# Kernel tuning notes

Measured on AMD Instinct MI355X. Metric: run time of the kernel, lower is better.

Reference implementation:

```python
import jax, jax.numpy as jnp
import numpy as np
import math

B, T, C, H = 4, 2048, 1024, 16
D = C // H  # head dim = 64


def setup_inputs() -> dict:
    key = jax.random.key(0)
    k1, k2, k3, k4, k5 = jax.random.split(key, 5)
    scale = 1.0 / math.sqrt(C)
    return {
        "x": jax.random.normal(k1, (B, T, C), dtype=jnp.float32),
        "w_attn": jax.random.normal(k2, (C, 3 * C), dtype=jnp.float32) * scale,
        "b_attn": jax.random.normal(k3, (3 * C,), dtype=jnp.float32) * 0.02,
        "w_proj": jax.random.normal(k4, (C, C), dtype=jnp.float32) * scale,
        "b_proj": jax.random.normal(k5, (C,), dtype=jnp.float32) * 0.02,
    }


def reference(x, w_attn, b_attn, w_proj, b_proj):
    Bx, Tx, Cx = x.shape
    qkv = x @ w_attn + b_attn                      # [B,T,3C]
    q, k, v = jnp.split(qkv, 3, axis=-1)           # each [B,T,C]
    # reshape to [B,H,T,D]
    q = q.reshape(Bx, Tx, H, D).transpose(0, 2, 1, 3)
    k = k.reshape(Bx, Tx, H, D).transpose(0, 2, 1, 3)
    v = v.reshape(Bx, Tx, H, D).transpose(0, 2, 1, 3)
    att = jnp.einsum("bhqd,bhkd->bhqk", q, k) * (1.0 / math.sqrt(D))
    causal = jnp.tril(jnp.ones((Tx, Tx), dtype=bool))
    att = jnp.where(causal, att, -jnp.inf)
    att = jax.nn.softmax(att, axis=-1)
    y = jnp.einsum("bhqk,bhkd->bhqd", att, v)      # [B,H,T,D]
    y = y.transpose(0, 2, 1, 3).reshape(Bx, Tx, Cx)
    return y @ w_proj + b_proj
```

## Files before the change

kernel.cpp:

```cpp
#include <hip/hip_runtime.h>
#include <hip/hip_bf16.h>
#include <stdint.h>

typedef unsigned short u16;
typedef unsigned int u32;
typedef __attribute__((ext_vector_type(8))) __bf16 bf16x8;
typedef __attribute__((ext_vector_type(4))) float f32x4;
typedef __attribute__((ext_vector_type(16))) float f32x16;

#define B_ 4
#define T_ 2048
#define C_ 1024
#define H_ 16
#define D_ 64

__device__ __forceinline__ u16 f2bf(float f) {
  union { float f; u32 u; } v; v.f = f;
  u32 r = (v.u + 0x7fffu + ((v.u >> 16) & 1u)) >> 16;
  return (u16)r;
}

__device__ __forceinline__ float fexp2(float x) {
  float r;
  asm("v_exp_f32 %0, %1\n\ts_nop 0" : "=v"(r) : "v"(x));
  return r;
}

__device__ __forceinline__ u32 cvtpk(float lo, float hi2) {
  u32 r;
  asm("v_cvt_pk_bf16_f32 %0, %1, %2" : "=v"(r) : "v"(lo), "v"(hi2));
  return r;
}

__device__ __forceinline__ void gll16(const void* g, void* l) {
  __builtin_amdgcn_global_load_lds((const __attribute__((address_space(1))) void*)g,
                                   (__attribute__((address_space(3))) void*)l, 16, 0, 0);
}

__global__ void k_convert(const float* __restrict__ src, u16* __restrict__ dst, int n4) {
  int stride = gridDim.x * blockDim.x;
  for (int i = blockIdx.x * blockDim.x + threadIdx.x; i < n4; i += stride) {
    float4 v = ((const float4*)src)[i];
    ushort4 o;
    o.x = f2bf(v.x); o.y = f2bf(v.y); o.z = f2bf(v.z); o.w = f2bf(v.w);
    ((ushort4*)dst)[i] = o;
  }
}

__global__ void k_transpose_bf16(const float* __restrict__ src, u16* __restrict__ dst,
                                 int K, int N) {
  __shared__ float tile[32][33];
  int k0 = blockIdx.x * 32, n0 = blockIdx.y * 32;
  int tx = threadIdx.x, ty = threadIdx.y;
#pragma unroll
  for (int r = 0; r < 4; ++r) {
    int k = ty + r * 8;
    tile[k][tx] = src[(size_t)(k0 + k) * N + n0 + tx];
  }
  __syncthreads();
#pragma unroll
  for (int r = 0; r < 4; ++r) {
    int n = ty + r * 8;
    dst[(size_t)(n0 + n) * K + k0 + tx] = f2bf(tile[tx][n]);
  }
}

template <int MODE>
__global__ __launch_bounds__(256) void k_gemm(
    const u16* __restrict__ A, const u16* __restrict__ BT, const float* __restrict__ bias,
    float* __restrict__ outF, u16* __restrict__ qb, u16* __restrict__ kb, u16* __restrict__ vbT,
    int M, int N, int K) {
  __shared__ u16 al[3][128 * 32];
  __shared__ u16 bl[3][128 * 32];
  const int lane = threadIdx.x & 63, wid = threadIdx.x >> 6;
  const int brow = blockIdx.y * 128, bcol = blockIdx.x * 128;
  const int wr = (wid >> 1) * 64, wc = (wid & 1) * 64;
  const int lr = lane & 15, lg = lane >> 4, lk = lg * 8;
  f32x4 acc[4][4] = {};

  auto stage = [&](u16* ad, u16* bd, int t2) {
    const int kt = t2 * 32;
#pragma unroll
    for (int it = 0; it < 2; ++it) {
      int cbase = (wid * 2 + it) * 64;
      int c = cbase + lane;
      int row = c >> 2, col = (c & 3) * 8;
      gll16(A + (size_t)(brow + row) * K + kt + col, ad + cbase * 8);
      gll16(BT + (size_t)(bcol + row) * K + kt + col, bd + cbase * 8);
    }
  };

  const int nt = K / 32;
  stage(al[0], bl[0], 0);
  stage(al[1], bl[1], 1);

  for (int t = 0; t < nt; ++t) {
    if (t == nt - 1) { asm volatile("s_waitcnt vmcnt(0)" ::: "memory"); }
    else             { asm volatile("s_waitcnt vmcnt(4)" ::: "memory"); }
    __builtin_amdgcn_sched_barrier(0);
    __builtin_amdgcn_s_barrier();
    __builtin_amdgcn_sched_barrier(0);

    const int nxt = t + 2;
    if (nxt < nt) {
      const int ib = nxt % 3;
      stage(al[ib], bl[ib], nxt);
    }

    const u16* ab = al[t % 3];
    const u16* bb = bl[t % 3];
    bf16x8 af[4], bfr[4];
#pragma unroll
    for (int m = 0; m < 4; ++m) af[m] = *(const bf16x8*)&ab[(wr + m * 16 + lr) * 32 + lk];
#pragma unroll
    for (int n = 0; n < 4; ++n) bfr[n] = *(const bf16x8*)&bb[(wc + n * 16 + lr) * 32 + lk];

    asm volatile("s_waitcnt lgkmcnt(0)" ::: "memory");
    __builtin_amdgcn_sched_barrier(0);
    __builtin_amdgcn_s_setprio(1);
#pragma unroll
    for (int m = 0; m < 4; ++m)
#pragma unroll
      for (int n = 0; n < 4; ++n)
        acc[m][n] = __builtin_amdgcn_mfma_f32_16x16x32_bf16(af[m], bfr[n], acc[m][n], 0, 0, 0);
    __builtin_amdgcn_s_setprio(0);
  }

#pragma unroll
  for (int m = 0; m < 4; ++m) {
    int row = brow + wr + m * 16 + lg * 4;
#pragma unroll
    for (int n = 0; n < 4; ++n) {
      int col = bcol + wc + n * 16 + lr;
      float bs = bias[col];
      if (MODE == 0) {
#pragma unroll
        for (int r = 0; r < 4; ++r)
          outF[(size_t)(row + r) * N + col] = acc[m][n][r] + bs;
      } else {
        int sec = col >> 10, cc = col & 1023;
        int h = cc >> 6, dd = cc & 63;
        int b = row >> 11, t = row & 2047;
        size_t bh = (size_t)(b * H_ + h);
        if (sec < 2) {
          u16* dst = (sec == 0 ? qb : kb) + (bh * T_ + t) * D_ + dd;
#pragma unroll
          for (int r = 0; r < 4; ++r) dst[(size_t)r * D_] = f2bf(acc[m][n][r] + bs);
        } else {
          ushort4 pk;
          pk.x = f2bf(acc[m][n][0] + bs);
          pk.y = f2bf(acc[m][n][1] + bs);
          pk.z = f2bf(acc[m][n][2] + bs);
          pk.w = f2bf(acc[m][n][3] + bs);
          *(ushort4*)&vbT[(bh * D_ + dd) * T_ + t] = pk;
        }
      }
    }
  }
}

__global__ __launch_bounds__(256) void k_attn(
    const u16* __restrict__ qb, const u16* __restrict__ kb,
    const u16* __restrict__ vbT, u16* __restrict__ attb) {
  __shared__ u16 kl0[64 * 64], kl1[64 * 64];
  __shared__ u16 vl0[64 * 64], vl1[64 * 64];
  const int lane = threadIdx.x & 63, wid = threadIdx.x >> 6;
  const int w = blockIdx.x;
  const int lid = (w & 7) * 64 + (w >> 3);
  const int bh = lid >> 3, qpair = lid & 7;
  const int b = bh >> 4, h = bh & 15;
  const int l31 = lane & 31, hi = lane >> 5;
  const int sw3 = l31 & 7;

  const float SC = 0.18033688f;

  const u16* kbase = kb + (size_t)bh * T_ * D_;
  const u16* vbase = vbT + (size_t)bh * D_ * T_;

  auto stage = [&](u16* kd, u16* vd, int kt) {
    const int k0 = kt * 64;
#pragma unroll
    for (int it = 0; it < 2; ++it) {
      int cbase = (wid * 2 + it) * 64;
      int c = cbase + lane;
      int cs = (c & ~7) | ((c ^ (c >> 3)) & 7);
      gll16(kbase + (size_t)k0 * D_ + (size_t)cs * 8, kd + cbase * 8);
      int vrow = cs >> 3, vcol = (cs & 7) * 8;
      gll16(vbase + (size_t)vrow * T_ + k0 + vcol, vd + cbase * 8);
    }
  };

  auto pack = [&](const f32x16& s, bf16x8* out) {
#pragma unroll
    for (int cc = 0; cc < 2; ++cc) {
      const int rb = cc * 8;
      u32 a  = cvtpk(s[rb + 0], s[rb + 1]);
      u32 c  = cvtpk(s[rb + 2], s[rb + 3]);
      u32 bb = cvtpk(s[rb + 4], s[rb + 5]);
      u32 d  = cvtpk(s[rb + 6], s[rb + 7]);
      u32 as = __shfl_xor(a, 32, 64), cs = __shfl_xor(c, 32, 64);
      u32 bs = __shfl_xor(bb, 32, 64), ds = __shfl_xor(d, 32, 64);
      union { u32 u[4]; bf16x8 v; } t;
      t.u[0] = hi ? bs : a;
      t.u[1] = hi ? ds : c;
      t.u[2] = hi ? bb : as;
      t.u[3] = hi ? d : cs;
      out[cc] = t.v;
    }
  };

#pragma unroll 1
  for (int pass = 0; pass < 2; ++pass) {
    const int qbk = pass ? (15 - qpair) : qpair;
    const int qw = qbk * 128 + wid * 32;

    const u16* qrow = qb + ((size_t)bh * T_ + qw + l31) * D_ + hi * 8;
    bf16x8 qf[4];
#pragma unroll
    for (int j = 0; j < 4; ++j) qf[j] = *(const bf16x8*)(qrow + j * 16);

    float lsum = 0.f;
    f32x16 o0 = {}, o1 = {};

    const int nt = 2 * qbk + 2;
    const int lastkt = (qw + 31) >> 6;

    auto compute = [&](const u16* kl, const u16* vl, int kt) {
      const int k0 = kt * 64;
      f32x16 s0 = {}, s1 = {};
      __builtin_amdgcn_s_setprio(1);
#pragma unroll
      for (int j = 0; j < 4; ++j) {
        const int ch = ((2 * j + hi) ^ sw3) << 3;
        const bf16x8 kf0 = *(const bf16x8*)&kl[l31 * 64 + ch];
        const bf16x8 kf1 = *(const bf16x8*)&kl[(l31 + 32) * 64 + ch];
        s0 = __builtin_amdgcn_mfma_f32_32x32x16_bf16(kf0, qf[j], s0, 0, 0, 0);
        s1 = __builtin_amdgcn_mfma_f32_32x32x16_bf16(kf1, qf[j], s1, 0, 0, 0);
      }
      __builtin_amdgcn_s_setprio(0);

      if (kt == lastkt) {
        const int q = qw + l31;
#pragma unroll
        for (int r = 0; r < 16; ++r) {
          const int kv = k0 + (r & 3) + 8 * (r >> 2) + 4 * hi;
          if (kv > q) s0[r] = -3e38f;
          if (kv + 32 > q) s1[r] = -3e38f;
        }
      }

#pragma unroll
      for (int r = 0; r < 16; ++r) s0[r] = fexp2(s0[r] * SC);
      float t0[8];
#pragma unroll
      for (int r = 0; r < 8; ++r) t0[r] = s0[r] + s0[r + 8];
#pragma unroll
      for (int w2 = 4; w2 >= 1; w2 >>= 1)
#pragma unroll
        for (int r = 0; r < 4; ++r)
          if (r < w2) t0[r] += t0[r + w2];

      bf16x8 pb0[2];
      pack(s0, pb0);
      __builtin_amdgcn_s_setprio(1);
#pragma unroll
      for (int c = 0; c < 2; ++c) {
        const int ch = ((2 * c + hi) ^ sw3) << 3;
        const bf16x8 vf0 = *(const bf16x8*)&vl[l31 * 64 + ch];
        const bf16x8 vf1 = *(const bf16x8*)&vl[(l31 + 32) * 64 + ch];
        o0 = __builtin_amdgcn_mfma_f32_32x32x16_bf16(vf0, pb0[c], o0, 0, 0, 0);
        o1 = __builtin_amdgcn_mfma_f32_32x32x16_bf16(vf1, pb0[c], o1, 0, 0, 0);
      }
      __builtin_amdgcn_s_setprio(0);

#pragma unroll
      for (int r = 0; r < 16; ++r) s1[r] = fexp2(s1[r] * SC);
      float t1[8];
#pragma unroll
      for (int r = 0; r < 8; ++r) t1[r] = s1[r] + s1[r + 8];
#pragma unroll
      for (int w2 = 4; w2 >= 1; w2 >>= 1)
#pragma unroll
        for (int r = 0; r < 4; ++r)
          if (r < w2) t1[r] += t1[r + w2];

      bf16x8 pb1[2];
      pack(s1, pb1);
      __builtin_amdgcn_s_setprio(1);
#pragma unroll
      for (int c = 2; c < 4; ++c) {
        const int ch = ((2 * c + hi) ^ sw3) << 3;
        const bf16x8 vf0 = *(const bf16x8*)&vl[l31 * 64 + ch];
        const bf16x8 vf1 = *(const bf16x8*)&vl[(l31 + 32) * 64 + ch];
        o0 = __builtin_amdgcn_mfma_f32_32x32x16_bf16(vf0, pb1[c - 2], o0, 0, 0, 0);
        o1 = __builtin_amdgcn_mfma_f32_32x32x16_bf16(vf1, pb1[c - 2], o1, 0, 0, 0);
      }
      __builtin_amdgcn_s_setprio(0);

      float ps = t0[0] + t1[0];
      ps += __shfl_xor(ps, 32, 64);
      lsum += ps;
    };

    stage(kl0, vl0, 0);
    __syncthreads();
    int kt = 0;
    while (true) {
      if (kt + 1 < nt) stage(kl1, vl1, kt + 1);
      if (kt <= lastkt) compute(kl0, vl0, kt);
      __syncthreads();
      if (++kt >= nt) break;
      if (kt + 1 < nt) stage(kl0, vl0, kt + 1);
      if (kt <= lastkt) compute(kl1, vl1, kt);
      __syncthreads();
      if (++kt >= nt) break;
    }

    const float inv = 1.0f / lsum;
    u16* orow = attb + ((size_t)b * T_ + qw + l31) * C_ + h * D_;
#pragma unroll
    for (int rg = 0; rg < 4; ++rg) {
      ushort4 w0, w1;
      w0.x = f2bf(o0[rg * 4 + 0] * inv); w0.y = f2bf(o0[rg * 4 + 1] * inv);
      w0.z = f2bf(o0[rg * 4 + 2] * inv); w0.w = f2bf(o0[rg * 4 + 3] * inv);
      w1.x = f2bf(o1[rg * 4 + 0] * inv); w1.y = f2bf(o1[rg * 4 + 1] * inv);
      w1.z = f2bf(o1[rg * 4 + 2] * inv); w1.w = f2bf(o1[rg * 4 + 3] * inv);
      const int d0 = rg * 8 + hi * 4;
      *(ushort4*)(orow + d0) = w0;
      *(ushort4*)(orow + d0 + 32) = w1;
    }
  }
}

extern "C" void kernel_launch(void* const* d_in, const int* in_sizes, int n_in,
                              void* d_out, int out_size, void* d_ws, size_t ws_size,
                              hipStream_t stream) {
  const float* x = (const float*)d_in[0];
  const float* w_attn = (const float*)d_in[1];
  const float* b_attn = (const float*)d_in[2];
  const float* w_proj = (const float*)d_in[3];
  const float* b_proj = (const float*)d_in[4];
  float* out = (float*)d_out;

  char* ws = (char*)d_ws;
  const size_t MB = 1024 * 1024;
  u16* xb   = (u16*)(ws);
  u16* attb = xb;
  u16* waT  = (u16*)(ws + 16 * MB);
  u16* wpT  = (u16*)(ws + 22 * MB);
  u16* qb   = (u16*)(ws + 24 * MB);
  u16* kb   = (u16*)(ws + 40 * MB);
  u16* vbT  = (u16*)(ws + 56 * MB);

  k_convert<<<2048, 256, 0, stream>>>(x, xb, (B_ * T_ * C_) / 4);
  k_transpose_bf16<<<dim3(C_ / 32, 3 * C_ / 32), dim3(32, 8), 0, stream>>>(w_attn, waT, C_, 3 * C_);
  k_transpose_bf16<<<dim3(C_ / 32, C_ / 32), dim3(32, 8), 0, stream>>>(w_proj, wpT, C_, C_);

  k_gemm<1><<<dim3(3 * C_ / 128, (B_ * T_) / 128), 256, 0, stream>>>(
      xb, waT, b_attn, nullptr, qb, kb, vbT, B_ * T_, 3 * C_, C_);

  k_attn<<<512, 256, 0, stream>>>(qb, kb, vbT, attb);

  k_gemm<0><<<dim3(C_ / 128, (B_ * T_) / 128), 256, 0, stream>>>(
      attb, wpT, b_proj, out, nullptr, nullptr, nullptr, B_ * T_, C_, C_);
}
```

Measured before the change: 175.3 us.

## Enlarge GEMM tiles to 128x256 with 8 waves, swizzled LDS and XCD-aware block mapping

The GEMM kernel now uses 512-thread blocks that compute 128x256 output tiles with 8 waves, up from 256 threads and 128x128 tiles, so each staged A tile is reused across more columns. LDS staging uses an XOR-swizzled layout to cut bank conflicts on the fragment reads. A 1D grid is remapped so that consecutive block IDs on the same XCD cover neighbouring tiles, which should improve L2 reuse. The risks are fewer blocks (a tail effect on 256 CUs), more LDS per block, and a changed vmcnt wait count that must match the new number of loads per stage.

```diff
diff --git a/kernel.cpp b/kernel.cpp
--- a/kernel.cpp
+++ b/kernel.cpp
@@ -66,54 +66,73 @@
 }
 
 template <int MODE>
-__global__ __launch_bounds__(256) void k_gemm(
+__global__ __launch_bounds__(512, 4) void k_gemm(
     const u16* __restrict__ A, const u16* __restrict__ BT, const float* __restrict__ bias,
     float* __restrict__ outF, u16* __restrict__ qb, u16* __restrict__ kb, u16* __restrict__ vbT,
     int M, int N, int K) {
-  __shared__ u16 al[3][128 * 32];
-  __shared__ u16 bl[3][128 * 32];
-  const int lane = threadIdx.x & 63, wid = threadIdx.x >> 6;
-  const int brow = blockIdx.y * 128, bcol = blockIdx.x * 128;
-  const int wr = (wid >> 1) * 64, wc = (wid & 1) * 64;
-  const int lr = lane & 15, lg = lane >> 4, lk = lg * 8;
+  __shared__ u16 al[3][512 * 8];
+  __shared__ u16 bl[3][1024 * 8];
+  const int tid = threadIdx.x;
+  const int lane = tid & 63, wid = tid >> 6;
+  const int wm = wid >> 2, wn = wid & 3;
+  const int nbx = N >> 8;
+  const int cpx = ((M >> 7) * nbx) >> 3;
+  const int wg = blockIdx.x;
+  const int lid = (wg & 7) * cpx + (wg >> 3);
+  const int brow = (lid / nbx) * 128, bcol = (lid % nbx) * 256;
+  const int lr = lane & 15, lg = lane >> 4;
   f32x4 acc[4][4] = {};
 
-  auto stage = [&](u16* ad, u16* bd, int t2) {
+  auto stage = [&](int t2, int bi) {
     const int kt = t2 * 32;
+    {
+      int s = tid;
+      int line = s >> 3, jp = s & 7;
+      int j = jp ^ (line & 7);
+      int row = line * 2 + (j >> 2), kc = j & 3;
+      gll16(A + (size_t)(brow + row) * K + kt + kc * 8, &al[bi][(tid & ~63) * 8]);
+    }
 #pragma unroll
     for (int it = 0; it < 2; ++it) {
-      int cbase = (wid * 2 + it) * 64;
-      int c = cbase + lane;
-      int row = c >> 2, col = (c & 3) * 8;
-      gll16(A + (size_t)(brow + row) * K + kt + col, ad + cbase * 8);
-      gll16(BT + (size_t)(bcol + row) * K + kt + col, bd + cbase * 8);
+      int s = it * 512 + tid;
+      int line = s >> 3, jp = s & 7;
+      int j = jp ^ (line & 7);
+      int row = line * 2 + (j >> 2), kc = j & 3;
+      gll16(BT + (size_t)(bcol + row) * K + kt + kc * 8,
+            &bl[bi][(it * 512 + (tid & ~63)) * 8]);
     }
   };
 
   const int nt = K / 32;
-  stage(al[0], bl[0], 0);
-  stage(al[1], bl[1], 1);
+  stage(0, 0);
+  stage(1, 1);
 
   for (int t = 0; t < nt; ++t) {
     if (t == nt - 1) { asm volatile("s_waitcnt vmcnt(0)" ::: "memory"); }
-    else             { asm volatile("s_waitcnt vmcnt(4)" ::: "memory"); }
+    else             { asm volatile("s_waitcnt vmcnt(3)" ::: "memory"); }
     __builtin_amdgcn_sched_barrier(0);
     __builtin_amdgcn_s_barrier();
     __builtin_amdgcn_sched_barrier(0);
 
-    const int nxt = t + 2;
-    if (nxt < nt) {
-      const int ib = nxt % 3;
-      stage(al[ib], bl[ib], nxt);
-    }
-
-    const u16* ab = al[t % 3];
-    const u16* bb = bl[t % 3];
+    if (t + 2 < nt) stage(t + 2, (t + 2) % 3);
+
+    const u16* la = al[t % 3];
+    const u16* lb = bl[t % 3];
     bf16x8 af[4], bfr[4];
 #pragma unroll
-    for (int m = 0; m < 4; ++m) af[m] = *(const bf16x8*)&ab[(wr + m * 16 + lr) * 32 + lk];
-#pragma unroll
-    for (int n = 0; n < 4; ++n) bfr[n] = *(const bf16x8*)&bb[(wc + n * 16 + lr) * 32 + lk];
+    for (int m = 0; m < 4; ++m) {
+      int ar = wm * 64 + m * 16 + lr;
+      int line = ar >> 1;
+      int jp = (((ar & 1) << 2) | lg) ^ (line & 7);
+      af[m] = *(const bf16x8*)&la[(line * 8 + jp) * 8];
+    }
+#pragma unroll
+    for (int n = 0; n < 4; ++n) {
+      int br = wn * 64 + n * 16 + lr;
+      int line = br >> 1;
+      int jp = (((br & 1) << 2) | lg) ^ (line & 7);
+      bfr[n] = *(const bf16x8*)&lb[(line * 8 + jp) * 8];
+    }
 
     asm volatile("s_waitcnt lgkmcnt(0)" ::: "memory");
     __builtin_amdgcn_sched_barrier(0);
@@ -128,10 +147,10 @@
 
 #pragma unroll
   for (int m = 0; m < 4; ++m) {
-    int row = brow + wr + m * 16 + lg * 4;
+    int row = brow + wm * 64 + m * 16 + lg * 4;
 #pragma unroll
     for (int n = 0; n < 4; ++n) {
-      int col = bcol + wc + n * 16 + lr;
+      int col = bcol + wn * 64 + n * 16 + lr;
       float bs = bias[col];
       if (MODE == 0) {
 #pragma unroll
@@ -356,11 +375,11 @@
   k_transpose_bf16<<<dim3(C_ / 32, 3 * C_ / 32), dim3(32, 8), 0, stream>>>(w_attn, waT, C_, 3 * C_);
   k_transpose_bf16<<<dim3(C_ / 32, C_ / 32), dim3(32, 8), 0, stream>>>(w_proj, wpT, C_, C_);
 
-  k_gemm<1><<<dim3(3 * C_ / 128, (B_ * T_) / 128), 256, 0, stream>>>(
+  k_gemm<1><<<(8192 / 128) * (3 * C_ / 256), 512, 0, stream>>>(
       xb, waT, b_attn, nullptr, qb, kb, vbT, B_ * T_, 3 * C_, C_);
 
   k_attn<<<512, 256, 0, stream>>>(qb, kb, vbT, attb);
 
-  k_gemm<0><<<dim3(C_ / 128, (B_ * T_) / 128), 256, 0, stream>>>(
+  k_gemm<0><<<(8192 / 128) * (C_ / 256), 512, 0, stream>>>(
       attb, wpT, b_proj, out, nullptr, nullptr, nullptr, B_ * T_, C_, C_);
 }
```

Measured after the change: 180.5 us. 2.9% more time.
